# Performance work log

Hardware: AMD Instinct MI355X
Metric: run time of the kernel (lower is better)

The kernel has to match this reference:

```python
import jax, jax.numpy as jnp
import numpy as np

B, N, F = 65536, 3, 256
H1, H2, LATENT = 512, 512, 256
EPS = 1e-5


def setup_inputs() -> dict:
    key = jax.random.key(0)
    ks = jax.random.split(key, 8)
    s = 0.02
    return {
        "x": jax.random.normal(ks[0], (B, N, F), dtype=jnp.float32),
        "W1": jax.random.normal(ks[1], (F, H1), dtype=jnp.float32) * s,
        "b1": jnp.zeros((H1,), dtype=jnp.float32),
        "W2": jax.random.normal(ks[2], (H1, H2), dtype=jnp.float32) * s,
        "b2": jnp.zeros((H2,), dtype=jnp.float32),
        "W3": jax.random.normal(ks[3], (H2, LATENT), dtype=jnp.float32) * s,
        "b3": jnp.zeros((LATENT,), dtype=jnp.float32),
        "gamma": jnp.ones((LATENT,), dtype=jnp.float32),
        "beta": jnp.zeros((LATENT,), dtype=jnp.float32),
    }


def reference(x, W1, b1, W2, b2, W3, b3, gamma, beta):
    # pairwise node sums over the 3 fixed edges -> [3, B, F]
    e = jnp.stack([x[:, 0] + x[:, 1], x[:, 0] + x[:, 2], x[:, 1] + x[:, 2]], axis=0)
    # shared MLP (Linear+ReLU, Linear+ReLU)
    h = jax.nn.relu(jnp.einsum("ebf,fh->ebh", e, W1) + b1)
    h = jax.nn.relu(jnp.einsum("ebh,hk->ebk", h, W2) + b2)
    # sum-aggregate over edge dim -> [B, H2]
    agg = h.sum(axis=0)
    # final linear -> [B, LATENT]
    z = agg @ W3 + b3
    # BatchNorm1d in training mode: batch mean/var (biased)
    mu = z.mean(axis=0)
    var = z.var(axis=0)
    zhat = (z - mu) * jax.lax.rsqrt(var + EPS)
    return zhat * gamma + beta
```

## Files before the change

### kernel.cpp

```cpp
#include <hip/hip_runtime.h>
#include <hip/hip_bf16.h>
#include <stdint.h>

#define NROWS   65536
#define EPS     1e-5f
#define BM      32
#define NBLK    (NROWS / BM)

typedef __attribute__((ext_vector_type(8))) short short8;
typedef __attribute__((ext_vector_type(4))) float f32x4;

__device__ __forceinline__ unsigned short f2bf(float f) {
    unsigned u = __float_as_uint(f);
    unsigned r = (u + 0x7FFFu + ((u >> 16) & 1u)) >> 16;
    return (unsigned short)r;
}

__device__ __forceinline__ unsigned cvtpk(float lo, float hi) {
    unsigned r;
    asm("v_cvt_pk_bf16_f32 %0, %1, %2" : "=v"(r) : "v"(lo), "v"(hi));
    return r;
}

__device__ __forceinline__ float bf2f(unsigned short v) {
    return __uint_as_float(((unsigned)v) << 16);
}

__device__ __forceinline__ int cellb(int kg, int r) {
    return (((kg << 5) + r) << 4) ^ ((kg & 3) << 5);
}

__device__ __forceinline__ uint4 pack8(float4 a0, float4 a1, float4 b0, float4 b1) {
    uint4 pk;
    pk.x = cvtpk(a0.x + b0.x, a0.y + b0.y);
    pk.y = cvtpk(a0.z + b0.z, a0.w + b0.w);
    pk.z = cvtpk(a1.x + b1.x, a1.y + b1.y);
    pk.w = cvtpk(a1.z + b1.z, a1.w + b1.w);
    return pk;
}

__global__ void k_prep(const float* __restrict__ W1, const float* __restrict__ W2,
                       const float* __restrict__ W3,
                       unsigned short* __restrict__ w1p, unsigned short* __restrict__ w2p,
                       unsigned short* __restrict__ w3p) {
    int idx = blockIdx.x * 256 + threadIdx.x;
    if (idx < 131072) {
        int j = idx & 7, l = (idx >> 3) & 63, kt = (idx >> 9) & 7, tile = idx >> 12;
        int n = tile * 16 + (l & 15);
        int k = kt * 32 + (l >> 4) * 8 + j;
        w1p[idx] = f2bf(W1[k * 512 + n]);
    } else if (idx < 393216) {
        int i2 = idx - 131072;
        int j = i2 & 7, l = (i2 >> 3) & 63, kt = (i2 >> 9) & 15, tile = i2 >> 13;
        int n = tile * 16 + (l & 15);
        int k = kt * 32 + (l >> 4) * 8 + j;
        w2p[i2] = f2bf(W2[k * 512 + n]);
    } else if (idx < 524288) {
        int i3 = idx - 393216;
        int j = i3 & 7, l = (i3 >> 3) & 63, kt = (i3 >> 9) & 15, tile = i3 >> 13;
        int n = tile * 16 + (l & 15);
        int k = kt * 32 + (l >> 4) * 8 + j;
        w3p[i3] = f2bf(W3[k * 256 + n]);
    }
}

__global__ __launch_bounds__(512) __attribute__((amdgpu_waves_per_eu(2, 2)))
void k_fused(const float* __restrict__ x,
             const unsigned short* __restrict__ w1p,
             const unsigned short* __restrict__ w2p,
             const unsigned short* __restrict__ w3p,
             const float* __restrict__ b1, const float* __restrict__ b2,
             const float* __restrict__ b3,
             float* __restrict__ out,
             float* __restrict__ psum, float* __restrict__ psumsq) {
    __shared__ __align__(16) unsigned char smem[147456];
    unsigned char* h1b  = smem;
    unsigned char* ebb  = smem + 98304;
    unsigned char* aggb = smem + 98304;
    unsigned short* zbufB = (unsigned short*)smem;

    const int tid = threadIdx.x;
    const int w   = tid >> 6;
    const int l   = tid & 63;
    const int l15 = l & 15;
    const int lg  = l >> 4;
    const int blk = blockIdx.x;
    const int row0 = blk * BM;

    const int sr  = tid & 31;
    const int skg = tid >> 5;
    const float* xrow = x + (size_t)(row0 + sr) * 768;

    float bias1[4], bias2[4];
#pragma unroll
    for (int nt = 0; nt < 4; ++nt) {
        bias1[nt] = b1[w * 64 + nt * 16 + l15];
        bias2[nt] = b2[w * 64 + nt * 16 + l15];
    }
    float bias3[2];
#pragma unroll
    for (int nt = 0; nt < 2; ++nt) bias3[nt] = b3[w * 32 + nt * 16 + l15];

#pragma unroll
    for (int h = 0; h < 2; ++h) {
        int kg = skg + h * 16;
        float4 n0a = *(const float4*)(xrow + kg * 8);
        float4 n0b = *(const float4*)(xrow + kg * 8 + 4);
        float4 n1a = *(const float4*)(xrow + 256 + kg * 8);
        float4 n1b = *(const float4*)(xrow + 256 + kg * 8 + 4);
        float4 n2a = *(const float4*)(xrow + 512 + kg * 8);
        float4 n2b = *(const float4*)(xrow + 512 + kg * 8 + 4);
        *(uint4*)(ebb + cellb(kg, sr))         = pack8(n0a, n0b, n1a, n1b);
        *(uint4*)(ebb + 16384 + cellb(kg, sr)) = pack8(n0a, n0b, n2a, n2b);
        *(uint4*)(ebb + 32768 + cellb(kg, sr)) = pack8(n1a, n1b, n2a, n2b);
    }

    f32x4 c1[3][2][4];
#pragma unroll
    for (int e = 0; e < 3; ++e)
#pragma unroll
        for (int mt = 0; mt < 2; ++mt)
#pragma unroll
            for (int nt = 0; nt < 4; ++nt) c1[e][mt][nt] = (f32x4){0.f, 0.f, 0.f, 0.f};

    {
        short8 aP[3][2], aQ[3][2], bP[4], bQ[4];
#pragma unroll
        for (int nt = 0; nt < 4; ++nt)
            bP[nt] = *(const short8*)(w1p + (((w * 4 + nt) * 8) * 64 + l) * 8);
        __syncthreads();
#pragma unroll
        for (int e = 0; e < 3; ++e)
#pragma unroll
            for (int mt = 0; mt < 2; ++mt)
                aP[e][mt] = *(const short8*)(ebb + e * 16384 + cellb(lg, mt * 16 + l15));
#pragma unroll 1
        for (int kt = 0; kt < 8; kt += 2) {
#pragma unroll
            for (int e = 0; e < 3; ++e)
#pragma unroll
                for (int mt = 0; mt < 2; ++mt)
                    aQ[e][mt] = *(const short8*)(ebb + e * 16384 + cellb((kt + 1) * 4 + lg, mt * 16 + l15));
#pragma unroll
            for (int nt = 0; nt < 4; ++nt)
                bQ[nt] = *(const short8*)(w1p + (((w * 4 + nt) * 8 + kt + 1) * 64 + l) * 8);
            __builtin_amdgcn_s_setprio(1);
#pragma unroll
            for (int nt = 0; nt < 4; ++nt)
#pragma unroll
                for (int e = 0; e < 3; ++e)
#pragma unroll
                    for (int mt = 0; mt < 2; ++mt)
                        c1[e][mt][nt] = __builtin_amdgcn_mfma_f32_16x16x32_bf16(aP[e][mt], bP[nt], c1[e][mt][nt], 0, 0, 0);
            __builtin_amdgcn_s_setprio(0);
            if (kt + 2 < 8) {
#pragma unroll
                for (int e = 0; e < 3; ++e)
#pragma unroll
                    for (int mt = 0; mt < 2; ++mt)
                        aP[e][mt] = *(const short8*)(ebb + e * 16384 + cellb((kt + 2) * 4 + lg, mt * 16 + l15));
#pragma unroll
                for (int nt = 0; nt < 4; ++nt)
                    bP[nt] = *(const short8*)(w1p + (((w * 4 + nt) * 8 + kt + 2) * 64 + l) * 8);
            }
            __builtin_amdgcn_s_setprio(1);
#pragma unroll
            for (int nt = 0; nt < 4; ++nt)
#pragma unroll
                for (int e = 0; e < 3; ++e)
#pragma unroll
                    for (int mt = 0; mt < 2; ++mt)
                        c1[e][mt][nt] = __builtin_amdgcn_mfma_f32_16x16x32_bf16(aQ[e][mt], bQ[nt], c1[e][mt][nt], 0, 0, 0);
            __builtin_amdgcn_s_setprio(0);
        }
    }

#pragma unroll
    for (int e = 0; e < 3; ++e)
#pragma unroll
        for (int nt = 0; nt < 4; ++nt) {
            int c = w * 64 + nt * 16 + l15;
            int cb = ((c & 7) << 1);
            unsigned char* base = h1b + e * 32768;
#pragma unroll
            for (int mt = 0; mt < 2; ++mt) {
                int r0 = mt * 16 + lg * 4;
                float v0 = fmaxf(c1[e][mt][nt][0] + bias1[nt], 0.f);
                float v1 = fmaxf(c1[e][mt][nt][1] + bias1[nt], 0.f);
                float v2 = fmaxf(c1[e][mt][nt][2] + bias1[nt], 0.f);
                float v3 = fmaxf(c1[e][mt][nt][3] + bias1[nt], 0.f);
                unsigned p01 = cvtpk(v0, v1);
                unsigned p23 = cvtpk(v2, v3);
                *(unsigned short*)(base + cellb(c >> 3, r0 + 0) + cb) = (unsigned short)p01;
                *(unsigned short*)(base + cellb(c >> 3, r0 + 1) + cb) = (unsigned short)(p01 >> 16);
                *(unsigned short*)(base + cellb(c >> 3, r0 + 2) + cb) = (unsigned short)p23;
                *(unsigned short*)(base + cellb(c >> 3, r0 + 3) + cb) = (unsigned short)(p23 >> 16);
            }
        }
    __syncthreads();

    f32x4 c2[3][2][4];
#pragma unroll
    for (int e = 0; e < 3; ++e)
#pragma unroll
        for (int mt = 0; mt < 2; ++mt)
#pragma unroll
            for (int nt = 0; nt < 4; ++nt) c2[e][mt][nt] = (f32x4){0.f, 0.f, 0.f, 0.f};

    {
        short8 aP[3][2], aQ[3][2], bP[4], bQ[4];
#pragma unroll
        for (int nt = 0; nt < 4; ++nt)
            bP[nt] = *(const short8*)(w2p + (((w * 4 + nt) * 16) * 64 + l) * 8);
#pragma unroll
        for (int e = 0; e < 3; ++e)
#pragma unroll
            for (int mt = 0; mt < 2; ++mt)
                aP[e][mt] = *(const short8*)(h1b + e * 32768 + cellb(lg, mt * 16 + l15));
#pragma unroll 1
        for (int kt = 0; kt < 16; kt += 2) {
#pragma unroll
            for (int e = 0; e < 3; ++e)
#pragma unroll
                for (int mt = 0; mt < 2; ++mt)
                    aQ[e][mt] = *(const short8*)(h1b + e * 32768 + cellb((kt + 1) * 4 + lg, mt * 16 + l15));
#pragma unroll
            for (int nt = 0; nt < 4; ++nt)
                bQ[nt] = *(const short8*)(w2p + (((w * 4 + nt) * 16 + kt + 1) * 64 + l) * 8);
            __builtin_amdgcn_s_setprio(1);
#pragma unroll
            for (int nt = 0; nt < 4; ++nt)
#pragma unroll
                for (int e = 0; e < 3; ++e)
#pragma unroll
                    for (int mt = 0; mt < 2; ++mt)
                        c2[e][mt][nt] = __builtin_amdgcn_mfma_f32_16x16x32_bf16(aP[e][mt], bP[nt], c2[e][mt][nt], 0, 0, 0);
            __builtin_amdgcn_s_setprio(0);
            if (kt + 2 < 16) {
#pragma unroll
                for (int e = 0; e < 3; ++e)
#pragma unroll
                    for (int mt = 0; mt < 2; ++mt)
                        aP[e][mt] = *(const short8*)(h1b + e * 32768 + cellb((kt + 2) * 4 + lg, mt * 16 + l15));
#pragma unroll
                for (int nt = 0; nt < 4; ++nt)
                    bP[nt] = *(const short8*)(w2p + (((w * 4 + nt) * 16 + kt + 2) * 64 + l) * 8);
            }
            __builtin_amdgcn_s_setprio(1);
#pragma unroll
            for (int nt = 0; nt < 4; ++nt)
#pragma unroll
                for (int e = 0; e < 3; ++e)
#pragma unroll
                    for (int mt = 0; mt < 2; ++mt)
                        c2[e][mt][nt] = __builtin_amdgcn_mfma_f32_16x16x32_bf16(aQ[e][mt], bQ[nt], c2[e][mt][nt], 0, 0, 0);
            __builtin_amdgcn_s_setprio(0);
        }
    }

#pragma unroll
    for (int nt = 0; nt < 4; ++nt) {
        int c = w * 64 + nt * 16 + l15;
        int cb = ((c & 7) << 1);
#pragma unroll
        for (int mt = 0; mt < 2; ++mt) {
            int r0 = mt * 16 + lg * 4;
            float s0 = 0.f, s1 = 0.f, s2 = 0.f, s3 = 0.f;
#pragma unroll
            for (int e = 0; e < 3; ++e) {
                s0 += fmaxf(c2[e][mt][nt][0] + bias2[nt], 0.f);
                s1 += fmaxf(c2[e][mt][nt][1] + bias2[nt], 0.f);
                s2 += fmaxf(c2[e][mt][nt][2] + bias2[nt], 0.f);
                s3 += fmaxf(c2[e][mt][nt][3] + bias2[nt], 0.f);
            }
            unsigned p01 = cvtpk(s0, s1);
            unsigned p23 = cvtpk(s2, s3);
            *(unsigned short*)(aggb + cellb(c >> 3, r0 + 0) + cb) = (unsigned short)p01;
            *(unsigned short*)(aggb + cellb(c >> 3, r0 + 1) + cb) = (unsigned short)(p01 >> 16);
            *(unsigned short*)(aggb + cellb(c >> 3, r0 + 2) + cb) = (unsigned short)p23;
            *(unsigned short*)(aggb + cellb(c >> 3, r0 + 3) + cb) = (unsigned short)(p23 >> 16);
        }
    }
    __syncthreads();

    f32x4 c3[2][2];
#pragma unroll
    for (int mt = 0; mt < 2; ++mt)
#pragma unroll
        for (int nt = 0; nt < 2; ++nt) c3[mt][nt] = (f32x4){0.f, 0.f, 0.f, 0.f};

    {
        short8 aP[2], aQ[2], bP[2], bQ[2];
#pragma unroll
        for (int nt = 0; nt < 2; ++nt)
            bP[nt] = *(const short8*)(w3p + (((w * 2 + nt) * 16) * 64 + l) * 8);
#pragma unroll
        for (int mt = 0; mt < 2; ++mt)
            aP[mt] = *(const short8*)(aggb + cellb(lg, mt * 16 + l15));
#pragma unroll 1
        for (int kt = 0; kt < 16; kt += 2) {
#pragma unroll
            for (int mt = 0; mt < 2; ++mt)
                aQ[mt] = *(const short8*)(aggb + cellb((kt + 1) * 4 + lg, mt * 16 + l15));
#pragma unroll
            for (int nt = 0; nt < 2; ++nt)
                bQ[nt] = *(const short8*)(w3p + (((w * 2 + nt) * 16 + kt + 1) * 64 + l) * 8);
            __builtin_amdgcn_s_setprio(1);
#pragma unroll
            for (int nt = 0; nt < 2; ++nt)
#pragma unroll
                for (int mt = 0; mt < 2; ++mt)
                    c3[mt][nt] = __builtin_amdgcn_mfma_f32_16x16x32_bf16(aP[mt], bP[nt], c3[mt][nt], 0, 0, 0);
            __builtin_amdgcn_s_setprio(0);
            if (kt + 2 < 16) {
#pragma unroll
                for (int mt = 0; mt < 2; ++mt)
                    aP[mt] = *(const short8*)(aggb + cellb((kt + 2) * 4 + lg, mt * 16 + l15));
#pragma unroll
                for (int nt = 0; nt < 2; ++nt)
                    bP[nt] = *(const short8*)(w3p + (((w * 2 + nt) * 16 + kt + 2) * 64 + l) * 8);
            }
            __builtin_amdgcn_s_setprio(1);
#pragma unroll
            for (int nt = 0; nt < 2; ++nt)
#pragma unroll
                for (int mt = 0; mt < 2; ++mt)
                    c3[mt][nt] = __builtin_amdgcn_mfma_f32_16x16x32_bf16(aQ[mt], bQ[nt], c3[mt][nt], 0, 0, 0);
            __builtin_amdgcn_s_setprio(0);
        }
    }

#pragma unroll
    for (int nt = 0; nt < 2; ++nt) {
        int c = w * 32 + nt * 16 + l15;
        float s = 0.f, q = 0.f;
#pragma unroll
        for (int mt = 0; mt < 2; ++mt) {
            int r0 = mt * 16 + lg * 4;
            float v0 = c3[mt][nt][0] + bias3[nt];
            float v1 = c3[mt][nt][1] + bias3[nt];
            float v2 = c3[mt][nt][2] + bias3[nt];
            float v3 = c3[mt][nt][3] + bias3[nt];
            unsigned p01 = cvtpk(v0, v1);
            unsigned p23 = cvtpk(v2, v3);
            zbufB[(r0 + 0) * 256 + c] = (unsigned short)p01;
            zbufB[(r0 + 1) * 256 + c] = (unsigned short)(p01 >> 16);
            zbufB[(r0 + 2) * 256 + c] = (unsigned short)p23;
            zbufB[(r0 + 3) * 256 + c] = (unsigned short)(p23 >> 16);
            s += v0 + v1 + v2 + v3;
            q += v0 * v0 + v1 * v1 + v2 * v2 + v3 * v3;
        }
        s += __shfl_xor(s, 16); s += __shfl_xor(s, 32);
        q += __shfl_xor(q, 16); q += __shfl_xor(q, 32);
        if (lg == 0) {
            psum[c * NBLK + blk] = s;
            psumsq[c * NBLK + blk] = q;
        }
    }
    __syncthreads();
    {
        const uint4* zb = (const uint4*)zbufB;
        char* ob = (char*)out;
#pragma unroll
        for (int it = 0; it < 2; ++it) {
            int j = tid + it * 512;
            int r = j >> 5, i = j & 31;
            *(uint4*)(ob + (size_t)(row0 + r) * 1024 + i * 16) = zb[j];
        }
    }
}

__global__ void k_stats2(const float* __restrict__ psum, const float* __restrict__ psumsq,
                         const float* __restrict__ gamma, const float* __restrict__ beta,
                         float* __restrict__ scale, float* __restrict__ shift) {
    int f = blockIdx.x, t = threadIdx.x;
    const float* ps = psum + f * NBLK;
    const float* pq = psumsq + f * NBLK;
    float s = 0.f, q = 0.f;
#pragma unroll
    for (int i = 0; i < 8; ++i) {
        s += ps[t + i * 256];
        q += pq[t + i * 256];
    }
#pragma unroll
    for (int o = 32; o > 0; o >>= 1) {
        s += __shfl_down(s, o);
        q += __shfl_down(q, o);
    }
    __shared__ float ls[4], lq[4];
    if ((t & 63) == 0) { ls[t >> 6] = s; lq[t >> 6] = q; }
    __syncthreads();
    if (t == 0) {
        s = ls[0] + ls[1] + ls[2] + ls[3];
        q = lq[0] + lq[1] + lq[2] + lq[3];
        float mu  = s * (1.f / 65536.f);
        float var = q * (1.f / 65536.f) - mu * mu;
        float sc  = gamma[f] * rsqrtf(var + EPS);
        scale[f] = sc;
        shift[f] = beta[f] - mu * sc;
    }
}

__global__ void k_norm(float* out, const float* __restrict__ scale,
                       const float* __restrict__ shift) {
    const int tid = threadIdx.x;
    const size_t row0 = (size_t)blockIdx.x * 32;
    const char* ob = (const char*)out;

    short8 zv[4];
    int rr[4], ii[4];
#pragma unroll
    for (int it = 0; it < 4; ++it) {
        int j = tid + it * 256;
        rr[it] = j >> 5; ii[it] = j & 31;
        zv[it] = *(const short8*)(ob + (row0 + rr[it]) * 1024 + ii[it] * 16);
    }
    __syncthreads();

#pragma unroll
    for (int it = 0; it < 4; ++it) {
        int c0 = ii[it] * 8;
        float4 sc0 = *(const float4*)(scale + c0);
        float4 sc1 = *(const float4*)(scale + c0 + 4);
        float4 sh0 = *(const float4*)(shift + c0);
        float4 sh1 = *(const float4*)(shift + c0 + 4);
        float4 o0, o1;
        o0.x = bf2f((unsigned short)zv[it][0]) * sc0.x + sh0.x;
        o0.y = bf2f((unsigned short)zv[it][1]) * sc0.y + sh0.y;
        o0.z = bf2f((unsigned short)zv[it][2]) * sc0.z + sh0.z;
        o0.w = bf2f((unsigned short)zv[it][3]) * sc0.w + sh0.w;
        o1.x = bf2f((unsigned short)zv[it][4]) * sc1.x + sh1.x;
        o1.y = bf2f((unsigned short)zv[it][5]) * sc1.y + sh1.y;
        o1.z = bf2f((unsigned short)zv[it][6]) * sc1.z + sh1.z;
        o1.w = bf2f((unsigned short)zv[it][7]) * sc1.w + sh1.w;
        float* dst = out + (row0 + rr[it]) * 256 + c0;
        *(float4*)dst = o0;
        *(float4*)(dst + 4) = o1;
    }
}

extern "C" void kernel_launch(void* const* d_in, const int* in_sizes, int n_in,
                              void* d_out, int out_size, void* d_ws, size_t ws_size,
                              hipStream_t stream) {
    const float* x     = (const float*)d_in[0];
    const float* W1    = (const float*)d_in[1];
    const float* b1    = (const float*)d_in[2];
    const float* W2    = (const float*)d_in[3];
    const float* b2    = (const float*)d_in[4];
    const float* W3    = (const float*)d_in[5];
    const float* b3    = (const float*)d_in[6];
    const float* gamma = (const float*)d_in[7];
    const float* beta  = (const float*)d_in[8];

    char* ws = (char*)d_ws;
    unsigned short* w1p = (unsigned short*)(ws);
    unsigned short* w2p = (unsigned short*)(ws + 262144);
    unsigned short* w3p = (unsigned short*)(ws + 786432);
    float* psum   = (float*)(ws + 1048576);
    float* psumsq = (float*)(ws + 3145728);
    float* scale  = (float*)(ws + 5242880);
    float* shift  = (float*)(ws + 5243904);

    float* out = (float*)d_out;

    k_prep<<<2048, 256, 0, stream>>>(W1, W2, W3, w1p, w2p, w3p);
    k_fused<<<NBLK, 512, 0, stream>>>(x, w1p, w2p, w3p, b1, b2, b3, out, psum, psumsq);
    k_stats2<<<256, 256, 0, stream>>>(psum, psumsq, gamma, beta, scale, shift);
    k_norm<<<2048, 256, 0, stream>>>(out, scale, shift);
}
```

Measured before the change: 225.7 us.

## Shrink fused MLP tile to 16 rows with 4 waves and move stats to separate pass

Halves the row tile per block to 16 rows and uses 256 threads (4 waves), each computing 128 output columns for layers 1–2 and 64 columns for layer 3. Shared memory drops to 72KB so more blocks can reside per CU. Per-block BatchNorm partial sums are removed from the fused kernel and recomputed by a new k_stats1 pass that rereads the bf16 z values from the output buffer. Each weight fragment is now reused across fewer rows, and the extra pass adds a read of the intermediate output.

```diff
diff --git a/kernel.cpp b/kernel.cpp
--- a/kernel.cpp
+++ b/kernel.cpp
@@ -4,7 +4,7 @@
 
 #define NROWS   65536
 #define EPS     1e-5f
-#define BM      32
+#define BM      16
 #define NBLK    (NROWS / BM)
 
 typedef __attribute__((ext_vector_type(8))) short short8;
@@ -27,7 +27,7 @@
 }
 
 __device__ __forceinline__ int cellb(int kg, int r) {
-    return (((kg << 5) + r) << 4) ^ ((kg & 3) << 5);
+    return (((kg << 4) + r) << 4) ^ ((kg & 3) << 5);
 }
 
 __device__ __forceinline__ uint4 pack8(float4 a0, float4 a1, float4 b0, float4 b1) {
@@ -64,19 +64,18 @@
     }
 }
 
-__global__ __launch_bounds__(512) __attribute__((amdgpu_waves_per_eu(2, 2)))
+__global__ __launch_bounds__(256) __attribute__((amdgpu_waves_per_eu(2, 2)))
 void k_fused(const float* __restrict__ x,
              const unsigned short* __restrict__ w1p,
              const unsigned short* __restrict__ w2p,
              const unsigned short* __restrict__ w3p,
              const float* __restrict__ b1, const float* __restrict__ b2,
              const float* __restrict__ b3,
-             float* __restrict__ out,
-             float* __restrict__ psum, float* __restrict__ psumsq) {
-    __shared__ __align__(16) unsigned char smem[147456];
+             float* __restrict__ out) {
+    __shared__ __align__(16) unsigned char smem[73728];
     unsigned char* h1b  = smem;
-    unsigned char* ebb  = smem + 98304;
-    unsigned char* aggb = smem + 98304;
+    unsigned char* ebb  = smem + 49152;
+    unsigned char* aggb = smem + 49152;
     unsigned short* zbufB = (unsigned short*)smem;
 
     const int tid = threadIdx.x;
@@ -87,19 +86,9 @@
     const int blk = blockIdx.x;
     const int row0 = blk * BM;
 
-    const int sr  = tid & 31;
-    const int skg = tid >> 5;
+    const int sr  = tid & 15;
+    const int skg = tid >> 4;
     const float* xrow = x + (size_t)(row0 + sr) * 768;
-
-    float bias1[4], bias2[4];
-#pragma unroll
-    for (int nt = 0; nt < 4; ++nt) {
-        bias1[nt] = b1[w * 64 + nt * 16 + l15];
-        bias2[nt] = b2[w * 64 + nt * 16 + l15];
-    }
-    float bias3[2];
-#pragma unroll
-    for (int nt = 0; nt < 2; ++nt) bias3[nt] = b3[w * 32 + nt * 16 + l15];
 
 #pragma unroll
     for (int h = 0; h < 2; ++h) {
@@ -110,150 +99,183 @@
         float4 n1b = *(const float4*)(xrow + 256 + kg * 8 + 4);
         float4 n2a = *(const float4*)(xrow + 512 + kg * 8);
         float4 n2b = *(const float4*)(xrow + 512 + kg * 8 + 4);
-        *(uint4*)(ebb + cellb(kg, sr))         = pack8(n0a, n0b, n1a, n1b);
-        *(uint4*)(ebb + 16384 + cellb(kg, sr)) = pack8(n0a, n0b, n2a, n2b);
-        *(uint4*)(ebb + 32768 + cellb(kg, sr)) = pack8(n1a, n1b, n2a, n2b);
-    }
-
-    f32x4 c1[3][2][4];
+        *(uint4*)(ebb + cellb(kg, sr))        = pack8(n0a, n0b, n1a, n1b);
+        *(uint4*)(ebb + 8192 + cellb(kg, sr)) = pack8(n0a, n0b, n2a, n2b);
+        *(uint4*)(ebb + 16384 + cellb(kg, sr)) = pack8(n1a, n1b, n2a, n2b);
+    }
+
+    f32x4 c1[3][8];
 #pragma unroll
     for (int e = 0; e < 3; ++e)
 #pragma unroll
-        for (int mt = 0; mt < 2; ++mt)
-#pragma unroll
-            for (int nt = 0; nt < 4; ++nt) c1[e][mt][nt] = (f32x4){0.f, 0.f, 0.f, 0.f};
+        for (int nt = 0; nt < 8; ++nt) c1[e][nt] = (f32x4){0.f, 0.f, 0.f, 0.f};
 
     {
-        short8 aP[3][2], aQ[3][2], bP[4], bQ[4];
-#pragma unroll
-        for (int nt = 0; nt < 4; ++nt)
-            bP[nt] = *(const short8*)(w1p + (((w * 4 + nt) * 8) * 64 + l) * 8);
+        short8 aP[3], aQ[3], bP[8], bQ[8];
+#pragma unroll
+        for (int nt = 0; nt < 8; ++nt)
+            bP[nt] = *(const short8*)(w1p + (((w * 8 + nt) * 8) * 64 + l) * 8);
         __syncthreads();
 #pragma unroll
         for (int e = 0; e < 3; ++e)
-#pragma unroll
-            for (int mt = 0; mt < 2; ++mt)
-                aP[e][mt] = *(const short8*)(ebb + e * 16384 + cellb(lg, mt * 16 + l15));
+            aP[e] = *(const short8*)(ebb + e * 8192 + cellb(lg, l15));
 #pragma unroll 1
         for (int kt = 0; kt < 8; kt += 2) {
 #pragma unroll
             for (int e = 0; e < 3; ++e)
-#pragma unroll
-                for (int mt = 0; mt < 2; ++mt)
-                    aQ[e][mt] = *(const short8*)(ebb + e * 16384 + cellb((kt + 1) * 4 + lg, mt * 16 + l15));
-#pragma unroll
-            for (int nt = 0; nt < 4; ++nt)
-                bQ[nt] = *(const short8*)(w1p + (((w * 4 + nt) * 8 + kt + 1) * 64 + l) * 8);
-            __builtin_amdgcn_s_setprio(1);
-#pragma unroll
-            for (int nt = 0; nt < 4; ++nt)
-#pragma unroll
-                for (int e = 0; e < 3; ++e)
-#pragma unroll
-                    for (int mt = 0; mt < 2; ++mt)
-                        c1[e][mt][nt] = __builtin_amdgcn_mfma_f32_16x16x32_bf16(aP[e][mt], bP[nt], c1[e][mt][nt], 0, 0, 0);
+                aQ[e] = *(const short8*)(ebb + e * 8192 + cellb((kt + 1) * 4 + lg, l15));
+#pragma unroll
+            for (int nt = 0; nt < 8; ++nt)
+                bQ[nt] = *(const short8*)(w1p + (((w * 8 + nt) * 8 + kt + 1) * 64 + l) * 8);
+            __builtin_amdgcn_s_setprio(1);
+#pragma unroll
+            for (int nt = 0; nt < 8; ++nt)
+#pragma unroll
+                for (int e = 0; e < 3; ++e)
+                    c1[e][nt] = __builtin_amdgcn_mfma_f32_16x16x32_bf16(aP[e], bP[nt], c1[e][nt], 0, 0, 0);
             __builtin_amdgcn_s_setprio(0);
             if (kt + 2 < 8) {
 #pragma unroll
                 for (int e = 0; e < 3; ++e)
-#pragma unroll
-                    for (int mt = 0; mt < 2; ++mt)
-                        aP[e][mt] = *(const short8*)(ebb + e * 16384 + cellb((kt + 2) * 4 + lg, mt * 16 + l15));
-#pragma unroll
-                for (int nt = 0; nt < 4; ++nt)
-                    bP[nt] = *(const short8*)(w1p + (((w * 4 + nt) * 8 + kt + 2) * 64 + l) * 8);
+                    aP[e] = *(const short8*)(ebb + e * 8192 + cellb((kt + 2) * 4 + lg, l15));
+#pragma unroll
+                for (int nt = 0; nt < 8; ++nt)
+                    bP[nt] = *(const short8*)(w1p + (((w * 8 + nt) * 8 + kt + 2) * 64 + l) * 8);
             }
             __builtin_amdgcn_s_setprio(1);
 #pragma unroll
-            for (int nt = 0; nt < 4; ++nt)
-#pragma unroll
-                for (int e = 0; e < 3; ++e)
-#pragma unroll
-                    for (int mt = 0; mt < 2; ++mt)
-                        c1[e][mt][nt] = __builtin_amdgcn_mfma_f32_16x16x32_bf16(aQ[e][mt], bQ[nt], c1[e][mt][nt], 0, 0, 0);
-            __builtin_amdgcn_s_setprio(0);
-        }
-    }
-
+            for (int nt = 0; nt < 8; ++nt)
+#pragma unroll
+                for (int e = 0; e < 3; ++e)
+                    c1[e][nt] = __builtin_amdgcn_mfma_f32_16x16x32_bf16(aQ[e], bQ[nt], c1[e][nt], 0, 0, 0);
+            __builtin_amdgcn_s_setprio(0);
+        }
+    }
+
+#pragma unroll
+    for (int nt = 0; nt < 8; ++nt) {
+        int c = w * 128 + nt * 16 + l15;
+        int cb = ((c & 7) << 1);
+        float bias = b1[c];
+        int r0 = lg * 4;
+#pragma unroll
+        for (int e = 0; e < 3; ++e) {
+            unsigned char* base = h1b + e * 16384;
+            float v0 = fmaxf(c1[e][nt][0] + bias, 0.f);
+            float v1 = fmaxf(c1[e][nt][1] + bias, 0.f);
+            float v2 = fmaxf(c1[e][nt][2] + bias, 0.f);
+            float v3 = fmaxf(c1[e][nt][3] + bias, 0.f);
+            unsigned p01 = cvtpk(v0, v1);
+            unsigned p23 = cvtpk(v2, v3);
+            *(unsigned short*)(base + cellb(c >> 3, r0 + 0) + cb) = (unsigned short)p01;
+            *(unsigned short*)(base + cellb(c >> 3, r0 + 1) + cb) = (unsigned short)(p01 >> 16);
+            *(unsigned short*)(base + cellb(c >> 3, r0 + 2) + cb) = (unsigned short)p23;
+            *(unsigned short*)(base + cellb(c >> 3, r0 + 3) + cb) = (unsigned short)(p23 >> 16);
+        }
+    }
+    __syncthreads();
+
+    f32x4 c2[3][8];
 #pragma unroll
     for (int e = 0; e < 3; ++e)
 #pragma unroll
-        for (int nt = 0; nt < 4; ++nt) {
-            int c = w * 64 + nt * 16 + l15;
-            int cb = ((c & 7) << 1);
-            unsigned char* base = h1b + e * 32768;
-#pragma unroll
-            for (int mt = 0; mt < 2; ++mt) {
-                int r0 = mt * 16 + lg * 4;
-                float v0 = fmaxf(c1[e][mt][nt][0] + bias1[nt], 0.f);
-                float v1 = fmaxf(c1[e][mt][nt][1] + bias1[nt], 0.f);
-                float v2 = fmaxf(c1[e][mt][nt][2] + bias1[nt], 0.f);
-                float v3 = fmaxf(c1[e][mt][nt][3] + bias1[nt], 0.f);
-                unsigned p01 = cvtpk(v0, v1);
-                unsigned p23 = cvtpk(v2, v3);
-                *(unsigned short*)(base + cellb(c >> 3, r0 + 0) + cb) = (unsigned short)p01;
-                *(unsigned short*)(base + cellb(c >> 3, r0 + 1) + cb) = (unsigned short)(p01 >> 16);
-                *(unsigned short*)(base + cellb(c >> 3, r0 + 2) + cb) = (unsigned short)p23;
-                *(unsigned short*)(base + cellb(c >> 3, r0 + 3) + cb) = (unsigned short)(p23 >> 16);
-            }
-        }
-    __syncthreads();
-
-    f32x4 c2[3][2][4];
-#pragma unroll
-    for (int e = 0; e < 3; ++e)
-#pragma unroll
-        for (int mt = 0; mt < 2; ++mt)
-#pragma unroll
-            for (int nt = 0; nt < 4; ++nt) c2[e][mt][nt] = (f32x4){0.f, 0.f, 0.f, 0.f};
+        for (int nt = 0; nt < 8; ++nt) c2[e][nt] = (f32x4){0.f, 0.f, 0.f, 0.f};
 
     {
-        short8 aP[3][2], aQ[3][2], bP[4], bQ[4];
-#pragma unroll
-        for (int nt = 0; nt < 4; ++nt)
-            bP[nt] = *(const short8*)(w2p + (((w * 4 + nt) * 16) * 64 + l) * 8);
+        short8 aP[3], aQ[3], bP[8], bQ[8];
+#pragma unroll
+        for (int nt = 0; nt < 8; ++nt)
+            bP[nt] = *(const short8*)(w2p + (((w * 8 + nt) * 16) * 64 + l) * 8);
 #pragma unroll
         for (int e = 0; e < 3; ++e)
-#pragma unroll
-            for (int mt = 0; mt < 2; ++mt)
-                aP[e][mt] = *(const short8*)(h1b + e * 32768 + cellb(lg, mt * 16 + l15));
+            aP[e] = *(const short8*)(h1b + e * 16384 + cellb(lg, l15));
 #pragma unroll 1
         for (int kt = 0; kt < 16; kt += 2) {
 #pragma unroll
             for (int e = 0; e < 3; ++e)
-#pragma unroll
-                for (int mt = 0; mt < 2; ++mt)
-                    aQ[e][mt] = *(const short8*)(h1b + e * 32768 + cellb((kt + 1) * 4 + lg, mt * 16 + l15));
+                aQ[e] = *(const short8*)(h1b + e * 16384 + cellb((kt + 1) * 4 + lg, l15));
+#pragma unroll
+            for (int nt = 0; nt < 8; ++nt)
+                bQ[nt] = *(const short8*)(w2p + (((w * 8 + nt) * 16 + kt + 1) * 64 + l) * 8);
+            __builtin_amdgcn_s_setprio(1);
+#pragma unroll
+            for (int nt = 0; nt < 8; ++nt)
+#pragma unroll
+                for (int e = 0; e < 3; ++e)
+                    c2[e][nt] = __builtin_amdgcn_mfma_f32_16x16x32_bf16(aP[e], bP[nt], c2[e][nt], 0, 0, 0);
+            __builtin_amdgcn_s_setprio(0);
+            if (kt + 2 < 16) {
+#pragma unroll
+                for (int e = 0; e < 3; ++e)
+                    aP[e] = *(const short8*)(h1b + e * 16384 + cellb((kt + 2) * 4 + lg, l15));
+#pragma unroll
+                for (int nt = 0; nt < 8; ++nt)
+                    bP[nt] = *(const short8*)(w2p + (((w * 8 + nt) * 16 + kt + 2) * 64 + l) * 8);
+            }
+            __builtin_amdgcn_s_setprio(1);
+#pragma unroll
+            for (int nt = 0; nt < 8; ++nt)
+#pragma unroll
+                for (int e = 0; e < 3; ++e)
+                    c2[e][nt] = __builtin_amdgcn_mfma_f32_16x16x32_bf16(aQ[e], bQ[nt], c2[e][nt], 0, 0, 0);
+            __builtin_amdgcn_s_setprio(0);
+        }
+    }
+
+#pragma unroll
+    for (int nt = 0; nt < 8; ++nt) {
+        int c = w * 128 + nt * 16 + l15;
+        int cb = ((c & 7) << 1);
+        float bias = b2[c];
+        int r0 = lg * 4;
+        float s0 = 0.f, s1 = 0.f, s2 = 0.f, s3 = 0.f;
+#pragma unroll
+        for (int e = 0; e < 3; ++e) {
+            s0 += fmaxf(c2[e][nt][0] + bias, 0.f);
+            s1 += fmaxf(c2[e][nt][1] + bias, 0.f);
+            s2 += fmaxf(c2[e][nt][2] + bias, 0.f);
+            s3 += fmaxf(c2[e][nt][3] + bias, 0.f);
+        }
+        unsigned p01 = cvtpk(s0, s1);
+        unsigned p23 = cvtpk(s2, s3);
+        *(unsigned short*)(aggb + cellb(c >> 3, r0 + 0) + cb) = (unsigned short)p01;
+        *(unsigned short*)(aggb + cellb(c >> 3, r0 + 1) + cb) = (unsigned short)(p01 >> 16);
+        *(unsigned short*)(aggb + cellb(c >> 3, r0 + 2) + cb) = (unsigned short)p23;
+        *(unsigned short*)(aggb + cellb(c >> 3, r0 + 3) + cb) = (unsigned short)(p23 >> 16);
+    }
+    __syncthreads();
+
+    f32x4 c3[4];
+#pragma unroll
+    for (int nt = 0; nt < 4; ++nt) c3[nt] = (f32x4){0.f, 0.f, 0.f, 0.f};
+
+    {
+        short8 aP, aQ, bP[4], bQ[4];
+#pragma unroll
+        for (int nt = 0; nt < 4; ++nt)
+            bP[nt] = *(const short8*)(w3p + (((w * 4 + nt) * 16) * 64 + l) * 8);
+        aP = *(const short8*)(aggb + cellb(lg, l15));
+#pragma unroll 1
+        for (int kt = 0; kt < 16; kt += 2) {
+            aQ = *(const short8*)(aggb + cellb((kt + 1) * 4 + lg, l15));
 #pragma unroll
             for (int nt = 0; nt < 4; ++nt)
-                bQ[nt] = *(const short8*)(w2p + (((w * 4 + nt) * 16 + kt + 1) * 64 + l) * 8);
+                bQ[nt] = *(const short8*)(w3p + (((w * 4 + nt) * 16 + kt + 1) * 64 + l) * 8);
             __builtin_amdgcn_s_setprio(1);
 #pragma unroll
             for (int nt = 0; nt < 4; ++nt)
-#pragma unroll
-                for (int e = 0; e < 3; ++e)
-#pragma unroll
-                    for (int mt = 0; mt < 2; ++mt)
-                        c2[e][mt][nt] = __builtin_amdgcn_mfma_f32_16x16x32_bf16(aP[e][mt], bP[nt], c2[e][mt][nt], 0, 0, 0);
+                c3[nt] = __builtin_amdgcn_mfma_f32_16x16x32_bf16(aP, bP[nt], c3[nt], 0, 0, 0);
             __builtin_amdgcn_s_setprio(0);
             if (kt + 2 < 16) {
-#pragma unroll
-                for (int e = 0; e < 3; ++e)
-#pragma unroll
-                    for (int mt = 0; mt < 2; ++mt)
-                        aP[e][mt] = *(const short8*)(h1b + e * 32768 + cellb((kt + 2) * 4 + lg, mt * 16 + l15));
+                aP = *(const short8*)(aggb + cellb((kt + 2) * 4 + lg, l15));
 #pragma unroll
                 for (int nt = 0; nt < 4; ++nt)
-                    bP[nt] = *(const short8*)(w2p + (((w * 4 + nt) * 16 + kt + 2) * 64 + l) * 8);
+                    bP[nt] = *(const short8*)(w3p + (((w * 4 + nt) * 16 + kt + 2) * 64 + l) * 8);
             }
             __builtin_amdgcn_s_setprio(1);
 #pragma unroll
             for (int nt = 0; nt < 4; ++nt)
-#pragma unroll
-                for (int e = 0; e < 3; ++e)
-#pragma unroll
-                    for (int mt = 0; mt < 2; ++mt)
-                        c2[e][mt][nt] = __builtin_amdgcn_mfma_f32_16x16x32_bf16(aQ[e][mt], bQ[nt], c2[e][mt][nt], 0, 0, 0);
+                c3[nt] = __builtin_amdgcn_mfma_f32_16x16x32_bf16(aQ, bQ[nt], c3[nt], 0, 0, 0);
             __builtin_amdgcn_s_setprio(0);
         }
     }
@@ -261,101 +283,18 @@
 #pragma unroll
     for (int nt = 0; nt < 4; ++nt) {
         int c = w * 64 + nt * 16 + l15;
-        int cb = ((c & 7) << 1);
-#pragma unroll
-        for (int mt = 0; mt < 2; ++mt) {
-            int r0 = mt * 16 + lg * 4;
-            float s0 = 0.f, s1 = 0.f, s2 = 0.f, s3 = 0.f;
-#pragma unroll
-            for (int e = 0; e < 3; ++e) {
-                s0 += fmaxf(c2[e][mt][nt][0] + bias2[nt], 0.f);
-                s1 += fmaxf(c2[e][mt][nt][1] + bias2[nt], 0.f);
-                s2 += fmaxf(c2[e][mt][nt][2] + bias2[nt], 0.f);
-                s3 += fmaxf(c2[e][mt][nt][3] + bias2[nt], 0.f);
-            }
-            unsigned p01 = cvtpk(s0, s1);
-            unsigned p23 = cvtpk(s2, s3);
-            *(unsigned short*)(aggb + cellb(c >> 3, r0 + 0) + cb) = (unsigned short)p01;
-            *(unsigned short*)(aggb + cellb(c >> 3, r0 + 1) + cb) = (unsigned short)(p01 >> 16);
-            *(unsigned short*)(aggb + cellb(c >> 3, r0 + 2) + cb) = (unsigned short)p23;
-            *(unsigned short*)(aggb + cellb(c >> 3, r0 + 3) + cb) = (unsigned short)(p23 >> 16);
-        }
-    }
-    __syncthreads();
-
-    f32x4 c3[2][2];
-#pragma unroll
-    for (int mt = 0; mt < 2; ++mt)
-#pragma unroll
-        for (int nt = 0; nt < 2; ++nt) c3[mt][nt] = (f32x4){0.f, 0.f, 0.f, 0.f};
-
-    {
-        short8 aP[2], aQ[2], bP[2], bQ[2];
-#pragma unroll
-        for (int nt = 0; nt < 2; ++nt)
-            bP[nt] = *(const short8*)(w3p + (((w * 2 + nt) * 16) * 64 + l) * 8);
-#pragma unroll
-        for (int mt = 0; mt < 2; ++mt)
-            aP[mt] = *(const short8*)(aggb + cellb(lg, mt * 16 + l15));
-#pragma unroll 1
-        for (int kt = 0; kt < 16; kt += 2) {
-#pragma unroll
-            for (int mt = 0; mt < 2; ++mt)
-                aQ[mt] = *(const short8*)(aggb + cellb((kt + 1) * 4 + lg, mt * 16 + l15));
-#pragma unroll
-            for (int nt = 0; nt < 2; ++nt)
-                bQ[nt] = *(const short8*)(w3p + (((w * 2 + nt) * 16 + kt + 1) * 64 + l) * 8);
-            __builtin_amdgcn_s_setprio(1);
-#pragma unroll
-            for (int nt = 0; nt < 2; ++nt)
-#pragma unroll
-                for (int mt = 0; mt < 2; ++mt)
-                    c3[mt][nt] = __builtin_amdgcn_mfma_f32_16x16x32_bf16(aP[mt], bP[nt], c3[mt][nt], 0, 0, 0);
-            __builtin_amdgcn_s_setprio(0);
-            if (kt + 2 < 16) {
-#pragma unroll
-                for (int mt = 0; mt < 2; ++mt)
-                    aP[mt] = *(const short8*)(aggb + cellb((kt + 2) * 4 + lg, mt * 16 + l15));
-#pragma unroll
-                for (int nt = 0; nt < 2; ++nt)
-                    bP[nt] = *(const short8*)(w3p + (((w * 2 + nt) * 16 + kt + 2) * 64 + l) * 8);
-            }
-            __builtin_amdgcn_s_setprio(1);
-#pragma unroll
-            for (int nt = 0; nt < 2; ++nt)
-#pragma unroll
-                for (int mt = 0; mt < 2; ++mt)
-                    c3[mt][nt] = __builtin_amdgcn_mfma_f32_16x16x32_bf16(aQ[mt], bQ[nt], c3[mt][nt], 0, 0, 0);
-            __builtin_amdgcn_s_setprio(0);
-        }
-    }
-
-#pragma unroll
-    for (int nt = 0; nt < 2; ++nt) {
-        int c = w * 32 + nt * 16 + l15;
-        float s = 0.f, q = 0.f;
-#pragma unroll
-        for (int mt = 0; mt < 2; ++mt) {
-            int r0 = mt * 16 + lg * 4;
-            float v0 = c3[mt][nt][0] + bias3[nt];
-            float v1 = c3[mt][nt][1] + bias3[nt];
-            float v2 = c3[mt][nt][2] + bias3[nt];
-            float v3 = c3[mt][nt][3] + bias3[nt];
-            unsigned p01 = cvtpk(v0, v1);
-            unsigned p23 = cvtpk(v2, v3);
-            zbufB[(r0 + 0) * 256 + c] = (unsigned short)p01;
-            zbufB[(r0 + 1) * 256 + c] = (unsigned short)(p01 >> 16);
-            zbufB[(r0 + 2) * 256 + c] = (unsigned short)p23;
-            zbufB[(r0 + 3) * 256 + c] = (unsigned short)(p23 >> 16);
-            s += v0 + v1 + v2 + v3;
-            q += v0 * v0 + v1 * v1 + v2 * v2 + v3 * v3;
-        }
-        s += __shfl_xor(s, 16); s += __shfl_xor(s, 32);
-        q += __shfl_xor(q, 16); q += __shfl_xor(q, 32);
-        if (lg == 0) {
-            psum[c * NBLK + blk] = s;
-            psumsq[c * NBLK + blk] = q;
-        }
+        float bias = b3[c];
+        int r0 = lg * 4;
+        float v0 = c3[nt][0] + bias;
+        float v1 = c3[nt][1] + bias;
+        float v2 = c3[nt][2] + bias;
+        float v3 = c3[nt][3] + bias;
+        unsigned p01 = cvtpk(v0, v1);
+        unsigned p23 = cvtpk(v2, v3);
+        zbufB[(r0 + 0) * 256 + c] = (unsigned short)p01;
+        zbufB[(r0 + 1) * 256 + c] = (unsigned short)(p01 >> 16);
+        zbufB[(r0 + 2) * 256 + c] = (unsigned short)p23;
+        zbufB[(r0 + 3) * 256 + c] = (unsigned short)(p23 >> 16);
     }
     __syncthreads();
     {
@@ -363,10 +302,51 @@
         char* ob = (char*)out;
 #pragma unroll
         for (int it = 0; it < 2; ++it) {
-            int j = tid + it * 512;
+            int j = tid + it * 256;
             int r = j >> 5, i = j & 31;
             *(uint4*)(ob + (size_t)(row0 + r) * 1024 + i * 16) = zb[j];
         }
+    }
+}
+
+__global__ void k_stats1(const float* __restrict__ out,
+                         float* __restrict__ psum, float* __restrict__ psumsq) {
+    const int tid = threadIdx.x;
+    const int b = blockIdx.x;
+    const int cg = tid & 31;
+    const int rs = tid >> 5;
+    const char* ob = (const char*)out;
+
+    float s[8], q[8];
+#pragma unroll
+    for (int j = 0; j < 8; ++j) { s[j] = 0.f; q[j] = 0.f; }
+
+#pragma unroll 2
+    for (int it = 0; it < 8; ++it) {
+        int r = b * 64 + rs + it * 8;
+        short8 zv = *(const short8*)(ob + (size_t)r * 1024 + cg * 16);
+#pragma unroll
+        for (int j = 0; j < 8; ++j) {
+            float f = bf2f((unsigned short)zv[j]);
+            s[j] += f;
+            q[j] += f * f;
+        }
+    }
+    __shared__ float ls[256 * 8], lq[256 * 8];
+#pragma unroll
+    for (int j = 0; j < 8; ++j) { ls[tid * 8 + j] = s[j]; lq[tid * 8 + j] = q[j]; }
+    __syncthreads();
+    {
+        int cc = tid;
+        int g = cc >> 3, j = cc & 7;
+        float ss = 0.f, qq = 0.f;
+#pragma unroll
+        for (int rsl = 0; rsl < 8; ++rsl) {
+            ss += ls[(rsl * 32 + g) * 8 + j];
+            qq += lq[(rsl * 32 + g) * 8 + j];
+        }
+        psum[cc * 1024 + b] = ss;
+        psumsq[cc * 1024 + b] = qq;
     }
 }
 
@@ -374,11 +354,11 @@
                          const float* __restrict__ gamma, const float* __restrict__ beta,
                          float* __restrict__ scale, float* __restrict__ shift) {
     int f = blockIdx.x, t = threadIdx.x;
-    const float* ps = psum + f * NBLK;
-    const float* pq = psumsq + f * NBLK;
+    const float* ps = psum + f * 1024;
+    const float* pq = psumsq + f * 1024;
     float s = 0.f, q = 0.f;
 #pragma unroll
-    for (int i = 0; i < 8; ++i) {
+    for (int i = 0; i < 4; ++i) {
         s += ps[t + i * 256];
         q += pq[t + i * 256];
     }
@@ -457,14 +437,15 @@
     unsigned short* w2p = (unsigned short*)(ws + 262144);
     unsigned short* w3p = (unsigned short*)(ws + 786432);
     float* psum   = (float*)(ws + 1048576);
-    float* psumsq = (float*)(ws + 3145728);
-    float* scale  = (float*)(ws + 5242880);
-    float* shift  = (float*)(ws + 5243904);
+    float* psumsq = (float*)(ws + 2097152);
+    float* scale  = (float*)(ws + 3145728);
+    float* shift  = (float*)(ws + 3146752);
 
     float* out = (float*)d_out;
 
     k_prep<<<2048, 256, 0, stream>>>(W1, W2, W3, w1p, w2p, w3p);
-    k_fused<<<NBLK, 512, 0, stream>>>(x, w1p, w2p, w3p, b1, b2, b3, out, psum, psumsq);
+    k_fused<<<NBLK, 256, 0, stream>>>(x, w1p, w2p, w3p, b1, b2, b3, out);
+    k_stats1<<<1024, 256, 0, stream>>>(out, psum, psumsq);
     k_stats2<<<256, 256, 0, stream>>>(psum, psumsq, gamma, beta, scale, shift);
     k_norm<<<2048, 256, 0, stream>>>(out, scale, shift);
 }
```

Measured after the change: 256.6 us. +13.7%, slower.
